# Kernel optimization log

Hardware: AMD Instinct MI355X
Metric: run time of the kernel (lower is better)

The kernel has to match this reference:

```python
import jax, jax.numpy as jnp
import numpy as np

GAMMA = 1.0  # RBF kernel width (init kwarg gamma)
N_PAIRS = 8_388_608
N_LAYERS = 8


def setup_inputs() -> dict:
    key = jax.random.key(0)
    ks = jax.random.split(key, 12)
    inp = {
        "x": jax.random.normal(ks[0], (N_PAIRS, 2), dtype=jnp.float32),
        "y": jax.random.normal(ks[1], (N_PAIRS, 2), dtype=jnp.float32),
        # input layer (clip=False)
        "W0": jax.random.normal(ks[2], (2, 2), dtype=jnp.float32),
        "b0": jax.random.normal(ks[3], (2,), dtype=jnp.float32),
        "scale0": jax.random.uniform(ks[4], (2,), dtype=jnp.float32),
        "shift0": jax.random.normal(ks[5], (2,), dtype=jnp.float32),
        # hidden layers (weights/biases clipped to [-5, 5] at construction)
        "Ws": jnp.clip(jax.random.normal(ks[6], (N_LAYERS, 2, 2), dtype=jnp.float32), -5.0, 5.0),
        "bs": jnp.clip(jax.random.normal(ks[7], (N_LAYERS, 2), dtype=jnp.float32), -5.0, 5.0),
        "scales": jax.random.uniform(ks[8], (N_LAYERS, 2), dtype=jnp.float32),
        "shifts": jax.random.normal(ks[9], (N_LAYERS, 2), dtype=jnp.float32),
        # final head Linear(2, 1)
        "Wf": jax.random.normal(ks[10], (1, 2), dtype=jnp.float32),
        "bf": jax.random.normal(ks[11], (1,), dtype=jnp.float32),
    }
    return inp


def _fraud_net(z, W0, b0, scale0, shift0, Ws, bs, scales, shifts, Wf, bf):
    # input layer: tanh(Linear(2,2)) * scale + shift   (z: [N,2])
    z = jnp.tanh(z @ W0.T + b0) * scale0 + shift0

    def step(z, p):
        W, b, s, t = p
        return jnp.tanh(z @ W.T + b) * s + t, None

    z, _ = jax.lax.scan(step, z, (Ws, bs, scales, shifts))
    # final Linear(2, 1) then squeeze -> [N]
    return (z @ Wf.T + bf)[..., 0]


def reference(x, y, W0, b0, scale0, shift0, Ws, bs, scales, shifts, Wf, bf):
    diff = x - y  # [N, 2]
    rbf = jnp.exp(-GAMMA * jnp.sum(diff * diff, axis=-1))  # [N]
    fx = _fraud_net(x, W0, b0, scale0, shift0, Ws, bs, scales, shifts, Wf, bf)
    fy = _fraud_net(y, W0, b0, scale0, shift0, Ws, bs, scales, shifts, Wf, bf)
    return rbf * fx * fy  # [N]
```

## Files before the change

### kernel.cpp

```cpp
#include <hip/hip_runtime.h>

#define N_LAYERS 8

__device__ __forceinline__ float fast_tanh(float x) {
    x = fminf(15.0f, fmaxf(-15.0f, x));
    float e = __expf(2.0f * x);
    float r = __builtin_amdgcn_rcpf(e + 1.0f);
    return fmaf(-2.0f, r, 1.0f);
}

__device__ __forceinline__ void layer2(float& z0, float& z1,
                                       float w0, float w1, float w2, float w3,
                                       float b0, float b1,
                                       float s0, float s1,
                                       float t0, float t1) {
    float a0 = fast_tanh(fmaf(z0, w0, fmaf(z1, w1, b0)));
    float a1 = fast_tanh(fmaf(z0, w2, fmaf(z1, w3, b1)));
    z0 = fmaf(a0, s0, t0);
    z1 = fmaf(a1, s1, t1);
}

__global__ __launch_bounds__(256) void fraud_kernel(
    const float* __restrict__ x, const float* __restrict__ y,
    const float* __restrict__ pW0, const float* __restrict__ pb0,
    const float* __restrict__ ps0, const float* __restrict__ pt0,
    const float* __restrict__ pWs, const float* __restrict__ pbs,
    const float* __restrict__ pss, const float* __restrict__ pts,
    const float* __restrict__ pWf, const float* __restrict__ pbf,
    float* __restrict__ out, int n4)
{
    int tid = blockIdx.x * blockDim.x + threadIdx.x;
    if (tid >= n4) return;

    float W00 = pW0[0], W01 = pW0[1], W02 = pW0[2], W03 = pW0[3];
    float B00 = pb0[0], B01 = pb0[1];
    float S00 = ps0[0], S01 = ps0[1];
    float T00 = pt0[0], T01 = pt0[1];
    float Wf0 = pWf[0], Wf1 = pWf[1], BF = pbf[0];

    float WS[N_LAYERS][4], BS[N_LAYERS][2], SS[N_LAYERS][2], TS[N_LAYERS][2];
#pragma unroll
    for (int l = 0; l < N_LAYERS; ++l) {
        WS[l][0] = pWs[l * 4 + 0]; WS[l][1] = pWs[l * 4 + 1];
        WS[l][2] = pWs[l * 4 + 2]; WS[l][3] = pWs[l * 4 + 3];
        BS[l][0] = pbs[l * 2 + 0]; BS[l][1] = pbs[l * 2 + 1];
        SS[l][0] = pss[l * 2 + 0]; SS[l][1] = pss[l * 2 + 1];
        TS[l][0] = pts[l * 2 + 0]; TS[l][1] = pts[l * 2 + 1];
    }

    const float4* x4 = (const float4*)x;
    const float4* y4 = (const float4*)y;
    float4 xa = x4[2 * tid], xb = x4[2 * tid + 1];
    float4 ya = y4[2 * tid], yb = y4[2 * tid + 1];

    float zx0[4] = {xa.x, xa.z, xb.x, xb.z};
    float zx1[4] = {xa.y, xa.w, xb.y, xb.w};
    float zy0[4] = {ya.x, ya.z, yb.x, yb.z};
    float zy1[4] = {ya.y, ya.w, yb.y, yb.w};

    float r[4];
#pragma unroll
    for (int i = 0; i < 4; ++i) {
        float dx = zx0[i] - zy0[i];
        float dy = zx1[i] - zy1[i];
        r[i] = __expf(-fmaf(dx, dx, dy * dy));
    }

#pragma unroll
    for (int i = 0; i < 4; ++i) {
        layer2(zx0[i], zx1[i], W00, W01, W02, W03, B00, B01, S00, S01, T00, T01);
        layer2(zy0[i], zy1[i], W00, W01, W02, W03, B00, B01, S00, S01, T00, T01);
    }

#pragma unroll
    for (int l = 0; l < N_LAYERS; ++l) {
#pragma unroll
        for (int i = 0; i < 4; ++i) {
            layer2(zx0[i], zx1[i], WS[l][0], WS[l][1], WS[l][2], WS[l][3],
                   BS[l][0], BS[l][1], SS[l][0], SS[l][1], TS[l][0], TS[l][1]);
            layer2(zy0[i], zy1[i], WS[l][0], WS[l][1], WS[l][2], WS[l][3],
                   BS[l][0], BS[l][1], SS[l][0], SS[l][1], TS[l][0], TS[l][1]);
        }
    }

    float res[4];
#pragma unroll
    for (int i = 0; i < 4; ++i) {
        float fx = fmaf(zx0[i], Wf0, fmaf(zx1[i], Wf1, BF));
        float fy = fmaf(zy0[i], Wf0, fmaf(zy1[i], Wf1, BF));
        res[i] = r[i] * fx * fy;
    }
    ((float4*)out)[tid] = make_float4(res[0], res[1], res[2], res[3]);
}

extern "C" void kernel_launch(void* const* d_in, const int* in_sizes, int n_in,
                              void* d_out, int out_size, void* d_ws, size_t ws_size,
                              hipStream_t stream) {
    const float* x   = (const float*)d_in[0];
    const float* y   = (const float*)d_in[1];
    const float* W0  = (const float*)d_in[2];
    const float* b0  = (const float*)d_in[3];
    const float* s0  = (const float*)d_in[4];
    const float* t0  = (const float*)d_in[5];
    const float* Ws  = (const float*)d_in[6];
    const float* bs  = (const float*)d_in[7];
    const float* ss  = (const float*)d_in[8];
    const float* ts  = (const float*)d_in[9];
    const float* Wf  = (const float*)d_in[10];
    const float* bf  = (const float*)d_in[11];
    float* out = (float*)d_out;

    int n  = out_size;
    int n4 = n / 4;
    dim3 block(256);
    dim3 grid((n4 + block.x - 1) / block.x);
    hipLaunchKernelGGL(fraud_kernel, grid, block, 0, stream,
                       x, y, W0, b0, s0, t0, Ws, bs, ss, ts, Wf, bf, out, n4);
}
```

Baseline: 228.7 us.

## Fold affine params into next layer and batch tanh reciprocals

Adds a tiny prologue kernel that folds each layer's scale/shift into the following layer's weights and bias, pre-scaled by 2·log2(e), so tanh uses a bare exp2. Four tanh denominators share a single hardware reciprocal via a product trick, trading transcendental ops for extra multiplies. The aim is to cut per-element ALU and transcendental-unit work in this compute-bound kernel. In exchange it adds a second kernel launch and a slight risk of precision loss or overflow in the product of denominators.

Result: faster. 211.7 us (-7.4%).

```diff
diff --git a/kernel.cpp b/kernel.cpp
--- a/kernel.cpp
+++ b/kernel.cpp
@@ -1,52 +1,83 @@
 #include <hip/hip_runtime.h>
 
 #define N_LAYERS 8
+#define LOG2E2 2.8853900817779268f
+#define NLOG2E 1.4426950408889634f
 
-__device__ __forceinline__ float fast_tanh(float x) {
-    x = fminf(15.0f, fmaxf(-15.0f, x));
-    float e = __expf(2.0f * x);
-    float r = __builtin_amdgcn_rcpf(e + 1.0f);
-    return fmaf(-2.0f, r, 1.0f);
+#if __has_builtin(__builtin_amdgcn_exp2f)
+__device__ __forceinline__ float exp2_fast(float x) { return __builtin_amdgcn_exp2f(x); }
+#else
+__device__ __forceinline__ float exp2_fast(float x) { return __expf(0.6931471805599453f * x); }
+#endif
+
+__global__ void fold_params(const float* __restrict__ W0, const float* __restrict__ b0,
+                            const float* __restrict__ s0, const float* __restrict__ t0,
+                            const float* __restrict__ Ws, const float* __restrict__ bs,
+                            const float* __restrict__ ss, const float* __restrict__ ts,
+                            const float* __restrict__ Wf, const float* __restrict__ bf,
+                            float* __restrict__ fp) {
+    if (threadIdx.x == 0 && blockIdx.x == 0) {
+        fp[0] = LOG2E2 * W0[0]; fp[1] = LOG2E2 * W0[1];
+        fp[2] = LOG2E2 * W0[2]; fp[3] = LOG2E2 * W0[3];
+        fp[4] = LOG2E2 * b0[0]; fp[5] = LOG2E2 * b0[1];
+        for (int l = 0; l < N_LAYERS; ++l) {
+            float ps0 = (l == 0) ? s0[0] : ss[(l - 1) * 2 + 0];
+            float ps1 = (l == 0) ? s0[1] : ss[(l - 1) * 2 + 1];
+            float pt0 = (l == 0) ? t0[0] : ts[(l - 1) * 2 + 0];
+            float pt1 = (l == 0) ? t0[1] : ts[(l - 1) * 2 + 1];
+            const float* W = Ws + l * 4;
+            const float* b = bs + l * 2;
+            float* o = fp + 6 + l * 6;
+            o[0] = LOG2E2 * W[0] * ps0; o[1] = LOG2E2 * W[1] * ps1;
+            o[2] = LOG2E2 * W[2] * ps0; o[3] = LOG2E2 * W[3] * ps1;
+            o[4] = LOG2E2 * (W[0] * pt0 + W[1] * pt1 + b[0]);
+            o[5] = LOG2E2 * (W[2] * pt0 + W[3] * pt1 + b[1]);
+        }
+        fp[54] = Wf[0] * ss[14];
+        fp[55] = Wf[1] * ss[15];
+        fp[56] = Wf[0] * ts[14] + Wf[1] * ts[15] + bf[0];
+    }
 }
 
-__device__ __forceinline__ void layer2(float& z0, float& z1,
-                                       float w0, float w1, float w2, float w3,
-                                       float b0, float b1,
-                                       float s0, float s1,
-                                       float t0, float t1) {
-    float a0 = fast_tanh(fmaf(z0, w0, fmaf(z1, w1, b0)));
-    float a1 = fast_tanh(fmaf(z0, w2, fmaf(z1, w3, b1)));
-    z0 = fmaf(a0, s0, t0);
-    z1 = fmaf(a1, s1, t1);
+__device__ __forceinline__ void tanh4_log2(const float u[4], float t[4]) {
+    float d[4];
+#pragma unroll
+    for (int i = 0; i < 4; ++i)
+        d[i] = exp2_fast(fminf(u[i], 30.0f)) + 1.0f;
+    float p2 = d[0] * d[1];
+    float p3 = p2 * d[2];
+    float p4 = p3 * d[3];
+    float R = __builtin_amdgcn_rcpf(p4);
+    float i3 = R * p3;  R *= d[3];
+    float i2 = R * p2;  R *= d[2];
+    float i1 = R * d[0];
+    float i0 = R * d[1];
+    t[0] = fmaf(-2.0f, i0, 1.0f);
+    t[1] = fmaf(-2.0f, i1, 1.0f);
+    t[2] = fmaf(-2.0f, i2, 1.0f);
+    t[3] = fmaf(-2.0f, i3, 1.0f);
+}
+
+__device__ __forceinline__ void layer4(const float* __restrict__ o,
+                                       float a0[4], float a1[4]) {
+    float w0 = o[0], w1 = o[1], w2 = o[2], w3 = o[3], c0 = o[4], c1 = o[5];
+    float u0[4], u1[4];
+#pragma unroll
+    for (int i = 0; i < 4; ++i) {
+        u0[i] = fmaf(a0[i], w0, fmaf(a1[i], w1, c0));
+        u1[i] = fmaf(a0[i], w2, fmaf(a1[i], w3, c1));
+    }
+    tanh4_log2(u0, a0);
+    tanh4_log2(u1, a1);
 }
 
 __global__ __launch_bounds__(256) void fraud_kernel(
     const float* __restrict__ x, const float* __restrict__ y,
-    const float* __restrict__ pW0, const float* __restrict__ pb0,
-    const float* __restrict__ ps0, const float* __restrict__ pt0,
-    const float* __restrict__ pWs, const float* __restrict__ pbs,
-    const float* __restrict__ pss, const float* __restrict__ pts,
-    const float* __restrict__ pWf, const float* __restrict__ pbf,
+    const float* __restrict__ fp,
     float* __restrict__ out, int n4)
 {
     int tid = blockIdx.x * blockDim.x + threadIdx.x;
     if (tid >= n4) return;
-
-    float W00 = pW0[0], W01 = pW0[1], W02 = pW0[2], W03 = pW0[3];
-    float B00 = pb0[0], B01 = pb0[1];
-    float S00 = ps0[0], S01 = ps0[1];
-    float T00 = pt0[0], T01 = pt0[1];
-    float Wf0 = pWf[0], Wf1 = pWf[1], BF = pbf[0];
-
-    float WS[N_LAYERS][4], BS[N_LAYERS][2], SS[N_LAYERS][2], TS[N_LAYERS][2];
-#pragma unroll
-    for (int l = 0; l < N_LAYERS; ++l) {
-        WS[l][0] = pWs[l * 4 + 0]; WS[l][1] = pWs[l * 4 + 1];
-        WS[l][2] = pWs[l * 4 + 2]; WS[l][3] = pWs[l * 4 + 3];
-        BS[l][0] = pbs[l * 2 + 0]; BS[l][1] = pbs[l * 2 + 1];
-        SS[l][0] = pss[l * 2 + 0]; SS[l][1] = pss[l * 2 + 1];
-        TS[l][0] = pts[l * 2 + 0]; TS[l][1] = pts[l * 2 + 1];
-    }
 
     const float4* x4 = (const float4*)x;
     const float4* y4 = (const float4*)y;
@@ -63,31 +94,22 @@
     for (int i = 0; i < 4; ++i) {
         float dx = zx0[i] - zy0[i];
         float dy = zx1[i] - zy1[i];
-        r[i] = __expf(-fmaf(dx, dx, dy * dy));
+        r[i] = exp2_fast(-NLOG2E * fmaf(dx, dx, dy * dy));
     }
 
 #pragma unroll
-    for (int i = 0; i < 4; ++i) {
-        layer2(zx0[i], zx1[i], W00, W01, W02, W03, B00, B01, S00, S01, T00, T01);
-        layer2(zy0[i], zy1[i], W00, W01, W02, W03, B00, B01, S00, S01, T00, T01);
+    for (int l = 0; l <= N_LAYERS; ++l) {
+        const float* o = fp + l * 6;
+        layer4(o, zx0, zx1);
+        layer4(o, zy0, zy1);
     }
 
-#pragma unroll
-    for (int l = 0; l < N_LAYERS; ++l) {
-#pragma unroll
-        for (int i = 0; i < 4; ++i) {
-            layer2(zx0[i], zx1[i], WS[l][0], WS[l][1], WS[l][2], WS[l][3],
-                   BS[l][0], BS[l][1], SS[l][0], SS[l][1], TS[l][0], TS[l][1]);
-            layer2(zy0[i], zy1[i], WS[l][0], WS[l][1], WS[l][2], WS[l][3],
-                   BS[l][0], BS[l][1], SS[l][0], SS[l][1], TS[l][0], TS[l][1]);
-        }
-    }
-
+    float wf0 = fp[54], wf1 = fp[55], bf_ = fp[56];
     float res[4];
 #pragma unroll
     for (int i = 0; i < 4; ++i) {
-        float fx = fmaf(zx0[i], Wf0, fmaf(zx1[i], Wf1, BF));
-        float fy = fmaf(zy0[i], Wf0, fmaf(zy1[i], Wf1, BF));
+        float fx = fmaf(zx0[i], wf0, fmaf(zx1[i], wf1, bf_));
+        float fy = fmaf(zy0[i], wf0, fmaf(zy1[i], wf1, bf_));
         res[i] = r[i] * fx * fy;
     }
     ((float4*)out)[tid] = make_float4(res[0], res[1], res[2], res[3]);
@@ -96,24 +118,28 @@
 extern "C" void kernel_launch(void* const* d_in, const int* in_sizes, int n_in,
                               void* d_out, int out_size, void* d_ws, size_t ws_size,
                               hipStream_t stream) {
-    const float* x   = (const float*)d_in[0];
-    const float* y   = (const float*)d_in[1];
-    const float* W0  = (const float*)d_in[2];
-    const float* b0  = (const float*)d_in[3];
-    const float* s0  = (const float*)d_in[4];
-    const float* t0  = (const float*)d_in[5];
-    const float* Ws  = (const float*)d_in[6];
-    const float* bs  = (const float*)d_in[7];
-    const float* ss  = (const float*)d_in[8];
-    const float* ts  = (const float*)d_in[9];
-    const float* Wf  = (const float*)d_in[10];
-    const float* bf  = (const float*)d_in[11];
+    const float* x  = (const float*)d_in[0];
+    const float* y  = (const float*)d_in[1];
+    const float* W0 = (const float*)d_in[2];
+    const float* b0 = (const float*)d_in[3];
+    const float* s0 = (const float*)d_in[4];
+    const float* t0 = (const float*)d_in[5];
+    const float* Ws = (const float*)d_in[6];
+    const float* bs = (const float*)d_in[7];
+    const float* ss = (const float*)d_in[8];
+    const float* ts = (const float*)d_in[9];
+    const float* Wf = (const float*)d_in[10];
+    const float* bf = (const float*)d_in[11];
     float* out = (float*)d_out;
+    float* fp  = (float*)d_ws;
+
+    hipLaunchKernelGGL(fold_params, dim3(1), dim3(64), 0, stream,
+                       W0, b0, s0, t0, Ws, bs, ss, ts, Wf, bf, fp);
 
     int n  = out_size;
     int n4 = n / 4;
     dim3 block(256);
     dim3 grid((n4 + block.x - 1) / block.x);
     hipLaunchKernelGGL(fraud_kernel, grid, block, 0, stream,
-                       x, y, W0, b0, s0, t0, Ws, bs, ss, ts, Wf, bf, out, n4);
+                       x, y, fp, out, n4);
 }
```
